# Performance work log

Hardware: AMD Instinct MI355X
Metric: run time of the kernel (lower is better)

The kernel has to match this reference:

```python
import jax, jax.numpy as jnp
import numpy as np

NUM_USERS = 100000
NUM_BOOKS = 100000
N_EDGES = 2000000
HIDDEN = 64


def setup_inputs() -> dict:
    key = jax.random.key(0)
    k1, k2, k3, k4, k5 = jax.random.split(key, 5)
    z_user = jax.random.normal(k1, (NUM_USERS, HIDDEN), dtype=jnp.float32)
    z_books = jax.random.normal(k2, (NUM_BOOKS, HIDDEN), dtype=jnp.float32)
    edge_label_index = jax.random.randint(k3, (2, N_EDGES), 0, NUM_USERS, dtype=jnp.int64)
    # torch Linear weights: W has shape [out, in], y = x @ W.T + b
    W1 = jax.random.normal(k4, (HIDDEN, 2 * HIDDEN), dtype=jnp.float32) * (1.0 / np.sqrt(2 * HIDDEN))
    b1 = jnp.zeros((HIDDEN,), dtype=jnp.float32)
    W2 = jax.random.normal(k5, (1, HIDDEN), dtype=jnp.float32) * (1.0 / np.sqrt(HIDDEN))
    b2 = jnp.zeros((1,), dtype=jnp.float32)
    return {"z_user": z_user, "z_books": z_books, "edge_label_index": edge_label_index,
            "W1": W1, "b1": b1, "W2": W2, "b2": b2}


def reference(z_user, z_books, edge_label_index, W1, b1, W2, b2):
    row, col = edge_label_index[0], edge_label_index[1]
    # gather + concat: [E, 2*H]
    z = jnp.concatenate([z_user[row], z_books[col]], axis=-1)
    h = jax.nn.relu(z @ W1.T + b1)           # [E, H]
    out = h @ W2.T + b2                       # [E, 1]
    return out.reshape(-1)
```

## Files before the change

kernel.cpp:

```cpp
#include <hip/hip_runtime.h>
#include <hip/hip_bf16.h>
#include <stdint.h>

typedef __bf16 bf16x8 __attribute__((ext_vector_type(8)));
typedef float  f32x4  __attribute__((ext_vector_type(4)));

#define W1_ROWS 64
#define W1_K    128
#define W1_PAD  136

static __device__ inline bf16x8 cvt8(const float4 a, const float4 b) {
    bf16x8 r;
    r[0] = (__bf16)a.x; r[1] = (__bf16)a.y; r[2] = (__bf16)a.z; r[3] = (__bf16)a.w;
    r[4] = (__bf16)b.x; r[5] = (__bf16)b.y; r[6] = (__bf16)b.z; r[7] = (__bf16)b.w;
    return r;
}

struct Stage { float4 x0, x1, x2, x3, x4, x5, x6, x7; };

static __device__ inline void issue_gather(Stage& S,
                                           const float* __restrict__ zu,
                                           const float* __restrict__ zb,
                                           int r, int c, int quad) {
    const float4* up = (const float4*)(zu + (size_t)r * 64);
    const float4* vp = (const float4*)(zb + (size_t)c * 64);
    const int q2 = quad * 2;
    S.x0 = up[q2];     S.x1 = up[q2 + 1];
    S.x2 = up[q2 + 8]; S.x3 = up[q2 + 9];
    S.x4 = vp[q2];     S.x5 = vp[q2 + 1];
    S.x6 = vp[q2 + 8]; S.x7 = vp[q2 + 9];
}

__global__ __launch_bounds__(256, 4)
void edge_decoder_mfma(const float* __restrict__ zu,
                       const float* __restrict__ zb,
                       const int*   __restrict__ eidx,
                       const float* __restrict__ w1,
                       const float* __restrict__ b1,
                       const float* __restrict__ w2,
                       const float* __restrict__ b2,
                       float*       __restrict__ out,
                       const int nedges)
{
    __shared__ __bf16 w1s[W1_ROWS * W1_PAD];

    const int lane = threadIdx.x & 63;
    const int m    = lane & 15;
    const int quad = lane >> 4;

    for (int i = threadIdx.x; i < W1_ROWS * (W1_K / 8); i += blockDim.x) {
        const int n = i >> 4, c8 = i & 15;
        const float4* wr = (const float4*)(w1 + (size_t)n * W1_K + c8 * 8);
        *(bf16x8*)(&w1s[n * W1_PAD + c8 * 8]) = cvt8(wr[0], wr[1]);
    }
    __syncthreads();

    float w2v[4], b1v[4];
#pragma unroll
    for (int t = 0; t < 4; ++t) {
        w2v[t] = w2[t * 16 + m];
        b1v[t] = b1[t * 16 + m];
    }
    const float b2f = b2[0];

    const int* __restrict__ rowp = eidx;
    const int* __restrict__ colp = eidx + nedges;
    const int ngroups = (nedges + 15) >> 4;

    const int wavesPerBlock = blockDim.x >> 6;
    const int gwave = blockIdx.x * wavesPerBlock + (threadIdx.x >> 6);
    const int nw    = gridDim.x * wavesPerBlock;
    const int nw2   = nw << 1;

    const char* lbase = (const char*)w1s + m * (W1_PAD * 2) + quad * 16;

    auto load_idx = [&](int gg, int& r, int& c) {
        int e = (gg < ngroups) ? ((gg << 4) + m) : 0;
        if (e >= nedges) e = nedges - 1;
        r = rowp[e]; c = colp[e];
    };

    auto compute_store = [&](const Stage& S, int gg) {
        bf16x8 A[4];
        A[0] = cvt8(S.x0, S.x1); A[1] = cvt8(S.x2, S.x3);
        A[2] = cvt8(S.x4, S.x5); A[3] = cvt8(S.x6, S.x7);

        f32x4 acc[4];
#pragma unroll
        for (int t = 0; t < 4; ++t)
            acc[t] = (f32x4){b1v[t], b1v[t], b1v[t], b1v[t]};

#pragma unroll
        for (int s = 0; s < 4; ++s) {
#pragma unroll
            for (int t = 0; t < 4; ++t) {
                const bf16x8 bf = *(const bf16x8*)(lbase + t * (16 * W1_PAD * 2) + s * 64);
                acc[t] = __builtin_amdgcn_mfma_f32_16x16x32_bf16(A[s], bf, acc[t], 0, 0, 0);
            }
        }

        float p[4] = {0.f, 0.f, 0.f, 0.f};
#pragma unroll
        for (int t = 0; t < 4; ++t)
#pragma unroll
            for (int rr = 0; rr < 4; ++rr)
                p[rr] = fmaf(fmaxf(acc[t][rr], 0.f), w2v[t], p[rr]);

#pragma unroll
        for (int off = 8; off >= 1; off >>= 1)
#pragma unroll
            for (int rr = 0; rr < 4; ++rr)
                p[rr] += __shfl_xor(p[rr], off, 64);

        if (m == 0) {
            const int eo = (gg << 4) + quad * 4;
            if (eo + 3 < nedges) {
                float4 o;
                o.x = p[0] + b2f; o.y = p[1] + b2f;
                o.z = p[2] + b2f; o.w = p[3] + b2f;
                *(float4*)(out + eo) = o;
            } else {
#pragma unroll
                for (int rr = 0; rr < 4; ++rr)
                    if (eo + rr < nedges) out[eo + rr] = p[rr] + b2f;
            }
        }
    };

    int g = gwave;
    int r0, c0, r1, c1;
    Stage S0, S1;

    load_idx(g,      r0, c0);
    load_idx(g + nw, r1, c1);
    issue_gather(S0, zu, zb, r0, c0, quad);
    issue_gather(S1, zu, zb, r1, c1, quad);
    load_idx(g + nw2,      r0, c0);
    load_idx(g + nw2 + nw, r1, c1);

    for (; g < ngroups; g += nw2) {
        compute_store(S0, g);
        issue_gather(S0, zu, zb, r0, c0, quad);
        load_idx(g + nw2 + nw2, r0, c0);

        compute_store(S1, g + nw);
        issue_gather(S1, zu, zb, r1, c1, quad);
        load_idx(g + nw2 + nw2 + nw, r1, c1);
    }
}

extern "C" void kernel_launch(void* const* d_in, const int* in_sizes, int n_in,
                              void* d_out, int out_size, void* d_ws, size_t ws_size,
                              hipStream_t stream) {
    const float* zu = (const float*)d_in[0];
    const float* zb = (const float*)d_in[1];
    const int*   ei = (const int*)d_in[2];
    const float* w1 = (const float*)d_in[3];
    const float* b1 = (const float*)d_in[4];
    const float* w2 = (const float*)d_in[5];
    const float* b2 = (const float*)d_in[6];
    float* out = (float*)d_out;

    const int nedges = in_sizes[2] / 2;

    dim3 grid(2048), block(256);
    hipLaunchKernelGGL(edge_decoder_mfma, grid, block, 0, stream,
                       zu, zb, ei, w1, b1, w2, b2, out, nedges);
}
```

Baseline: 231.5 us.

## Pre-convert embedding tables to bf16 and keep W1 fragments in registers

Adds a pre-pass kernel that converts both embedding tables to bf16 in the workspace, so the edge kernel gathers 128-byte rows instead of 256-byte rows. The pre-pass reads 51 MB and writes 25.6 MB, and it runs on every call. W1 fragments now live in registers instead of LDS, and the 16-lane reduction uses DPP row adds instead of shuffles. If the workspace is too small, the code falls back to the fp32 gather path.

```diff
diff --git a/kernel.cpp b/kernel.cpp
--- a/kernel.cpp
+++ b/kernel.cpp
@@ -4,10 +4,6 @@
 
 typedef __bf16 bf16x8 __attribute__((ext_vector_type(8)));
 typedef float  f32x4  __attribute__((ext_vector_type(4)));
-
-#define W1_ROWS 64
-#define W1_K    128
-#define W1_PAD  136
 
 static __device__ inline bf16x8 cvt8(const float4 a, const float4 b) {
     bf16x8 r;
@@ -16,44 +12,98 @@
     return r;
 }
 
-struct Stage { float4 x0, x1, x2, x3, x4, x5, x6, x7; };
-
-static __device__ inline void issue_gather(Stage& S,
-                                           const float* __restrict__ zu,
-                                           const float* __restrict__ zb,
+template<int CTRL>
+static __device__ inline float dpp_add(float x) {
+    int y = __builtin_amdgcn_mov_dpp(__float_as_int(x), CTRL, 0xf, 0xf, true);
+    return x + __int_as_float(y);
+}
+static __device__ inline float row16_sum(float x) {
+    x = dpp_add<0x128>(x);
+    x = dpp_add<0x124>(x);
+    x = dpp_add<0x122>(x);
+    x = dpp_add<0x121>(x);
+    return x;
+}
+
+__global__ __launch_bounds__(256)
+void cvt_tables(const float* __restrict__ zu, const float* __restrict__ zb,
+                __bf16* __restrict__ ubf, __bf16* __restrict__ bbf,
+                const int n8u, const int n8b)
+{
+    int i = blockIdx.x * blockDim.x + threadIdx.x;
+    const int stride = gridDim.x * blockDim.x;
+    const int tot = n8u + n8b;
+    for (; i < tot; i += stride) {
+        const float* src; __bf16* dst; int j;
+        if (i < n8u) { src = zu; dst = ubf; j = i; }
+        else         { src = zb; dst = bbf; j = i - n8u; }
+        const float4* p = (const float4*)(src + (size_t)j * 8);
+        *(bf16x8*)(dst + (size_t)j * 8) = cvt8(p[0], p[1]);
+    }
+}
+
+template<bool BF> struct Stage;
+template<> struct Stage<true>  { bf16x8 a0, a1, a2, a3; };
+template<> struct Stage<false> { float4 x0,x1,x2,x3,x4,x5,x6,x7; };
+
+template<bool BF>
+static __device__ inline void issue_gather(Stage<BF>& S,
+                                           const void* __restrict__ zu,
+                                           const void* __restrict__ zb,
                                            int r, int c, int quad) {
-    const float4* up = (const float4*)(zu + (size_t)r * 64);
-    const float4* vp = (const float4*)(zb + (size_t)c * 64);
-    const int q2 = quad * 2;
-    S.x0 = up[q2];     S.x1 = up[q2 + 1];
-    S.x2 = up[q2 + 8]; S.x3 = up[q2 + 9];
-    S.x4 = vp[q2];     S.x5 = vp[q2 + 1];
-    S.x6 = vp[q2 + 8]; S.x7 = vp[q2 + 9];
-}
-
-__global__ __launch_bounds__(256, 4)
-void edge_decoder_mfma(const float* __restrict__ zu,
-                       const float* __restrict__ zb,
-                       const int*   __restrict__ eidx,
-                       const float* __restrict__ w1,
-                       const float* __restrict__ b1,
-                       const float* __restrict__ w2,
-                       const float* __restrict__ b2,
-                       float*       __restrict__ out,
-                       const int nedges)
+    if constexpr (BF) {
+        const char* up = (const char*)zu + ((size_t)r << 7) + quad * 16;
+        const char* vp = (const char*)zb + ((size_t)c << 7) + quad * 16;
+        S.a0 = *(const bf16x8*)(up);
+        S.a1 = *(const bf16x8*)(up + 64);
+        S.a2 = *(const bf16x8*)(vp);
+        S.a3 = *(const bf16x8*)(vp + 64);
+    } else {
+        const float4* up = (const float4*)((const float*)zu + ((size_t)r << 6));
+        const float4* vp = (const float4*)((const float*)zb + ((size_t)c << 6));
+        const int q2 = quad * 2;
+        S.x0 = up[q2];     S.x1 = up[q2 + 1];
+        S.x2 = up[q2 + 8]; S.x3 = up[q2 + 9];
+        S.x4 = vp[q2];     S.x5 = vp[q2 + 1];
+        S.x6 = vp[q2 + 8]; S.x7 = vp[q2 + 9];
+    }
+}
+
+template<bool BF>
+static __device__ inline void to_frags(const Stage<BF>& S, bf16x8 A[4]) {
+    if constexpr (BF) { A[0] = S.a0; A[1] = S.a1; A[2] = S.a2; A[3] = S.a3; }
+    else {
+        A[0] = cvt8(S.x0, S.x1); A[1] = cvt8(S.x2, S.x3);
+        A[2] = cvt8(S.x4, S.x5); A[3] = cvt8(S.x6, S.x7);
+    }
+}
+
+template<bool BF, int MINW>
+__global__ __launch_bounds__(256, MINW)
+void edge_decoder(const void* __restrict__ zu,
+                  const void* __restrict__ zb,
+                  const int*  __restrict__ eidx,
+                  const float* __restrict__ w1,
+                  const float* __restrict__ b1,
+                  const float* __restrict__ w2,
+                  const float* __restrict__ b2,
+                  float*      __restrict__ out,
+                  const int nedges)
 {
-    __shared__ __bf16 w1s[W1_ROWS * W1_PAD];
-
     const int lane = threadIdx.x & 63;
     const int m    = lane & 15;
     const int quad = lane >> 4;
 
-    for (int i = threadIdx.x; i < W1_ROWS * (W1_K / 8); i += blockDim.x) {
-        const int n = i >> 4, c8 = i & 15;
-        const float4* wr = (const float4*)(w1 + (size_t)n * W1_K + c8 * 8);
-        *(bf16x8*)(&w1s[n * W1_PAD + c8 * 8]) = cvt8(wr[0], wr[1]);
-    }
-    __syncthreads();
+    bf16x8 Bf[4][4];
+#pragma unroll
+    for (int t = 0; t < 4; ++t) {
+        const float4* wrow = (const float4*)(w1 + (size_t)(t * 16 + m) * 128);
+#pragma unroll
+        for (int s = 0; s < 4; ++s) {
+            const int c0 = s * 8 + quad * 2;
+            Bf[t][s] = cvt8(wrow[c0], wrow[c0 + 1]);
+        }
+    }
 
     float w2v[4], b1v[4];
 #pragma unroll
@@ -71,8 +121,6 @@
     const int gwave = blockIdx.x * wavesPerBlock + (threadIdx.x >> 6);
     const int nw    = gridDim.x * wavesPerBlock;
     const int nw2   = nw << 1;
-
-    const char* lbase = (const char*)w1s + m * (W1_PAD * 2) + quad * 16;
 
     auto load_idx = [&](int gg, int& r, int& c) {
         int e = (gg < ngroups) ? ((gg << 4) + m) : 0;
@@ -80,10 +128,9 @@
         r = rowp[e]; c = colp[e];
     };
 
-    auto compute_store = [&](const Stage& S, int gg) {
+    auto compute_store = [&](const Stage<BF>& S, int gg) {
         bf16x8 A[4];
-        A[0] = cvt8(S.x0, S.x1); A[1] = cvt8(S.x2, S.x3);
-        A[2] = cvt8(S.x4, S.x5); A[3] = cvt8(S.x6, S.x7);
+        to_frags<BF>(S, A);
 
         f32x4 acc[4];
 #pragma unroll
@@ -91,13 +138,10 @@
             acc[t] = (f32x4){b1v[t], b1v[t], b1v[t], b1v[t]};
 
 #pragma unroll
-        for (int s = 0; s < 4; ++s) {
-#pragma unroll
-            for (int t = 0; t < 4; ++t) {
-                const bf16x8 bf = *(const bf16x8*)(lbase + t * (16 * W1_PAD * 2) + s * 64);
-                acc[t] = __builtin_amdgcn_mfma_f32_16x16x32_bf16(A[s], bf, acc[t], 0, 0, 0);
-            }
-        }
+        for (int s = 0; s < 4; ++s)
+#pragma unroll
+            for (int t = 0; t < 4; ++t)
+                acc[t] = __builtin_amdgcn_mfma_f32_16x16x32_bf16(A[s], Bf[t][s], acc[t], 0, 0, 0);
 
         float p[4] = {0.f, 0.f, 0.f, 0.f};
 #pragma unroll
@@ -107,10 +151,8 @@
                 p[rr] = fmaf(fmaxf(acc[t][rr], 0.f), w2v[t], p[rr]);
 
 #pragma unroll
-        for (int off = 8; off >= 1; off >>= 1)
-#pragma unroll
-            for (int rr = 0; rr < 4; ++rr)
-                p[rr] += __shfl_xor(p[rr], off, 64);
+        for (int rr = 0; rr < 4; ++rr)
+            p[rr] = row16_sum(p[rr]);
 
         if (m == 0) {
             const int eo = (gg << 4) + quad * 4;
@@ -129,22 +171,22 @@
 
     int g = gwave;
     int r0, c0, r1, c1;
-    Stage S0, S1;
+    Stage<BF> S0, S1;
 
     load_idx(g,      r0, c0);
     load_idx(g + nw, r1, c1);
-    issue_gather(S0, zu, zb, r0, c0, quad);
-    issue_gather(S1, zu, zb, r1, c1, quad);
+    issue_gather<BF>(S0, zu, zb, r0, c0, quad);
+    issue_gather<BF>(S1, zu, zb, r1, c1, quad);
     load_idx(g + nw2,      r0, c0);
     load_idx(g + nw2 + nw, r1, c1);
 
     for (; g < ngroups; g += nw2) {
         compute_store(S0, g);
-        issue_gather(S0, zu, zb, r0, c0, quad);
+        issue_gather<BF>(S0, zu, zb, r0, c0, quad);
         load_idx(g + nw2 + nw2, r0, c0);
 
         compute_store(S1, g + nw);
-        issue_gather(S1, zu, zb, r1, c1, quad);
+        issue_gather<BF>(S1, zu, zb, r1, c1, quad);
         load_idx(g + nw2 + nw2 + nw, r1, c1);
     }
 }
@@ -162,8 +204,23 @@
     float* out = (float*)d_out;
 
     const int nedges = in_sizes[2] / 2;
+    const size_t nzu = (size_t)in_sizes[0];
+    const size_t nzb = (size_t)in_sizes[1];
+    const size_t need = (nzu + nzb) * sizeof(__bf16);
 
     dim3 grid(2048), block(256);
-    hipLaunchKernelGGL(edge_decoder_mfma, grid, block, 0, stream,
-                       zu, zb, ei, w1, b1, w2, b2, out, nedges);
-}
+
+    if (d_ws != nullptr && ws_size >= need) {
+        __bf16* ubf = (__bf16*)d_ws;
+        __bf16* bbf = ubf + nzu;
+        hipLaunchKernelGGL(cvt_tables, dim3(1024), block, 0, stream,
+                           zu, zb, ubf, bbf, (int)(nzu / 8), (int)(nzb / 8));
+        hipLaunchKernelGGL((edge_decoder<true, 3>), grid, block, 0, stream,
+                           (const void*)ubf, (const void*)bbf, ei, w1, b1, w2, b2,
+                           out, nedges);
+    } else {
+        hipLaunchKernelGGL((edge_decoder<false, 2>), grid, block, 0, stream,
+                           (const void*)zu, (const void*)zb, ei, w1, b1, w2, b2,
+                           out, nedges);
+    }
+}
```

Result: faster. 195.3 us (-15.7%).
